# Performance work log

Hardware: AMD Instinct MI355X
Metric: run time of the kernel (lower is better)

The kernel has to match this reference:

```python
import jax, jax.numpy as jnp
import numpy as np

ROLLBACK = 1  # rollback_range: warp at 2**rollback finer resolution, then downsample
B, C, H, W = 2, 32, 512, 512
CIN = 3 * (C // 2) + 2  # inner module input channels


def _bilinear_warp(img, res):
    """Bilinear gather. img: [B,Cc,Hh,Ww]; res: [B,Hh,Ww,2] pixel offsets (x,y).
    Samples img at (x+res_x, y+res_y) with zero padding outside."""
    Bb, Cc, Hh, Ww = img.shape
    gy, gx = jnp.meshgrid(jnp.arange(Hh, dtype=img.dtype),
                          jnp.arange(Ww, dtype=img.dtype), indexing='ij')
    sx = gx[None] + res[..., 0]  # [B,Hh,Ww]
    sy = gy[None] + res[..., 1]
    x0 = jnp.floor(sx); y0 = jnp.floor(sy)
    wx = sx - x0; wy = sy - y0

    def gather(yi, xi):
        inb = ((yi >= 0) & (yi < Hh) & (xi >= 0) & (xi < Ww)).astype(img.dtype)
        yc = jnp.clip(yi, 0, Hh - 1).astype(jnp.int32)
        xc = jnp.clip(xi, 0, Ww - 1).astype(jnp.int32)
        v = jax.vmap(lambda im, y, x: im[:, y, x])(img, yc, xc)  # [B,Cc,Hh,Ww]
        return v * inb[:, None]

    v00 = gather(y0, x0);     v01 = gather(y0, x0 + 1)
    v10 = gather(y0 + 1, x0); v11 = gather(y0 + 1, x0 + 1)
    wx = wx[:, None]; wy = wy[:, None]  # broadcast over channels
    return (v00 * (1 - wy) * (1 - wx) + v01 * (1 - wy) * wx
            + v10 * wy * (1 - wx) + v11 * wy * wx)


def _resize_img(img, f):  # [B,Cc,Hh,Ww] bilinear spatial resize
    Bb, Cc, Hh, Ww = img.shape
    return jax.image.resize(img, (Bb, Cc, int(Hh * f), int(Ww * f)), 'bilinear')


def _resize_res(res, f):  # [B,Hh,Ww,2]; pixel-unit values scale with resolution
    Bb, Hh, Ww, _ = res.shape
    return jax.image.resize(res, (Bb, int(Hh * f), int(Ww * f), 2), 'bilinear') * f


def res_warp_img(img, res, rollback):
    if rollback > 0:
        f = 2 ** rollback
        out = _bilinear_warp(_resize_img(img, f), _resize_res(res, f))
        return _resize_img(out, 1.0 / f)
    return _bilinear_warp(img, res)


def res_warp_res(res_a, res_b, rollback):
    # warp residual field a (treated as a 2-channel image, values in pixel units) by b
    if rollback > 0:
        f = 2 ** rollback
        a = _resize_res(res_a, f); b = _resize_res(res_b, f)
        out = jnp.transpose(_bilinear_warp(jnp.transpose(a, (0, 3, 1, 2)), b), (0, 2, 3, 1))
        return _resize_res(out, 1.0 / f)
    out = _bilinear_warp(jnp.transpose(res_a, (0, 3, 1, 2)), res_b)
    return jnp.transpose(out, (0, 2, 3, 1))


def combine_residuals(res_a, res_b, rollback):
    # flow composition: apply a then b
    return res_b + res_warp_res(res_a, res_b, rollback)


def _conv3x3(x, w, b):
    y = jax.lax.conv_general_dilated(x, w, (1, 1), 'SAME',
                                     dimension_numbers=('NCHW', 'OIHW', 'NCHW'))
    return y + b[None, :, None, None]


def setup_inputs() -> dict:
    key = jax.random.key(0)
    k1, k2, k3 = jax.random.split(key, 3)
    x = jax.random.normal(k1, (B, C, H, W), dtype=jnp.float32)
    res = jax.random.normal(k2, (B, 2, H, W), dtype=jnp.float32)  # ~1px flow
    W_inner = jax.random.normal(k3, (2, CIN, 3, 3), dtype=jnp.float32) * 0.02
    b_inner = jnp.zeros((2,), dtype=jnp.float32)
    return {"x": x, "res": res, "W_inner": W_inner, "b_inner": b_inner, "level": 0}


def reference(x, res, W_inner, b_inner, level):
    res_hw = jnp.transpose(res, (0, 2, 3, 1))  # [B,H,W,2]
    nf = x.shape[1]
    src, tgt = x[:, :nf // 2], x[:, nf // 2:]
    warped_tgt = res_warp_img(tgt, res_hw, ROLLBACK)
    bundle = jnp.concatenate([src, tgt, warped_tgt, res], axis=1)  # [B,3C/2+2,H,W]
    adj = _conv3x3(bundle, W_inner, b_inner)  # hindsight_adjustment [B,2,H,W]
    # mode == 'combine_res': state['down'][level]['input'] = combined residual
    new_res = combine_residuals(res_hw, jnp.transpose(adj, (0, 2, 3, 1)), ROLLBACK)
    hindsight_warped_tgt = res_warp_img(tgt, new_res, ROLLBACK)
    return jnp.concatenate([src, hindsight_warped_tgt], axis=1)  # [B,C,H,W]
```

## Files before the change

### kernel.cpp

```cpp
#include <hip/hip_runtime.h>
#include <hip/hip_bf16.h>
#include <cstdint>
#include <cstddef>

#define HW   512
#define HW2  1024
#define SZ   (512 * 512)
#define NPT  (34 * 34)
#define K_PTS 5
#define SRCW 36
#define NSRC (SRCW * SRCW)
#define MARG 9

struct UpTap { int i0, i1; float w0, w1; };

__device__ __forceinline__ UpTap up_tap(int i) {
  UpTap t;
  int k = i >> 1;
  if ((i & 1) == 0) {
    t.i0 = k - 1; t.i1 = k; t.w0 = 0.25f; t.w1 = 0.75f;
    if (k == 0) { t.i0 = 0; t.w0 = 0.0f; t.w1 = 1.0f; }
  } else {
    t.i0 = k; t.i1 = k + 1; t.w0 = 0.75f; t.w1 = 0.25f;
    if (k == HW - 1) { t.i1 = HW - 1; t.w0 = 1.0f; t.w1 = 0.0f; }
  }
  return t;
}

__device__ __forceinline__ float up_at(const float* __restrict__ plane, int yi, int xi) {
  UpTap ty = up_tap(yi), tx = up_tap(xi);
  const float* r0 = plane + (size_t)ty.i0 * HW;
  const float* r1 = plane + (size_t)ty.i1 * HW;
  float v00 = r0[tx.i0], v01 = r0[tx.i1];
  float v10 = r1[tx.i0], v11 = r1[tx.i1];
  return ty.w0 * (tx.w0 * v00 + tx.w1 * v01) + ty.w1 * (tx.w0 * v10 + tx.w1 * v11);
}

__device__ __forceinline__ void axis_taps(float s, int& base, float& w0, float& w1, float& w2) {
  float f0 = floorf(s);
  int i0 = (int)f0;
  float fr = s - f0;
  int b = (i0 & 1) ? (i0 >> 1) : (i0 >> 1) - 1;
  b = b < 0 ? 0 : (b > (HW - 3) ? (HW - 3) : b);
  float w[3] = {0.0f, 0.0f, 0.0f};
  if ((unsigned)i0 < (unsigned)HW2) {
    UpTap t = up_tap(i0);
    w[t.i0 - b] += (1.0f - fr) * t.w0;
    w[t.i1 - b] += (1.0f - fr) * t.w1;
  }
  if ((unsigned)(i0 + 1) < (unsigned)HW2) {
    UpTap t = up_tap(i0 + 1);
    w[t.i0 - b] += fr * t.w0;
    w[t.i1 - b] += fr * t.w1;
  }
  base = b; w0 = w[0]; w1 = w[1]; w2 = w[2];
}

struct PtTaps {
  int   locoff;
  float wy0, wy1, wy2, wx0, wx1, wx2;
};

__device__ __forceinline__ void compute_taps(const float* __restrict__ fx,
                                             const float* __restrict__ fy,
                                             int gx0, int gy0, int xo, int yo, int tid,
                                             PtTaps (&pt)[K_PTS]) {
  #pragma unroll
  for (int i = 0; i < K_PTS; ++i) {
    int p = tid + i * 256;
    pt[i].locoff = 0;
    pt[i].wy0 = pt[i].wy1 = pt[i].wy2 = 0.0f;
    pt[i].wx0 = pt[i].wx1 = pt[i].wx2 = 0.0f;
    if (p < NPT) {
      int ry = p / 34, rx = p % 34;
      int yy = gy0 + ry, xx = gx0 + rx;
      if ((unsigned)yy < (unsigned)HW2 && (unsigned)xx < (unsigned)HW2) {
        float sx = (float)xx + 2.0f * up_at(fx, yy, xx);
        float sy = (float)yy + 2.0f * up_at(fy, yy, xx);
        int bx, by;
        axis_taps(sx, bx, pt[i].wx0, pt[i].wx1, pt[i].wx2);
        axis_taps(sy, by, pt[i].wy0, pt[i].wy1, pt[i].wy2);
        int rx_ = bx - xo, ry_ = by - yo;
        if ((unsigned)rx_ <= (unsigned)(SRCW - 3) && (unsigned)ry_ <= (unsigned)(SRCW - 3))
          pt[i].locoff = ry_ * SRCW + rx_;
        else
          pt[i].locoff = ~(by * HW + bx);
      }
    }
  }
}

__device__ __forceinline__ void stage_pair(const float* __restrict__ p0,
                                           const float* __restrict__ p1,
                                           float2* __restrict__ s_src,
                                           int xo, int yo, int tid) {
  #pragma unroll
  for (int i = 0; i < 6; ++i) {
    int p = tid + i * 256;
    if (p < NSRC) {
      int r = p / SRCW, c = p % SRCW;
      int gy = yo + r; gy = gy < 0 ? 0 : (gy > HW - 1 ? HW - 1 : gy);
      int gx = xo + c; gx = gx < 0 ? 0 : (gx > HW - 1 ? HW - 1 : gx);
      size_t o = (size_t)gy * HW + gx;
      s_src[p] = make_float2(p0[o], p1[o]);
    }
  }
}

__device__ __forceinline__ float eval3_global(const float* __restrict__ pl, int off, const PtTaps& t) {
  const float* p0 = pl + off;
  float r0 = t.wx0 * p0[0]        + t.wx1 * p0[1]          + t.wx2 * p0[2];
  float r1 = t.wx0 * p0[HW]       + t.wx1 * p0[HW + 1]     + t.wx2 * p0[HW + 2];
  float r2 = t.wx0 * p0[2 * HW]   + t.wx1 * p0[2 * HW + 1] + t.wx2 * p0[2 * HW + 2];
  return t.wy0 * r0 + t.wy1 * r1 + t.wy2 * r2;
}

__device__ __forceinline__ void eval_round(const float2* __restrict__ s_src,
                                           float2* __restrict__ s_tile,
                                           const float* __restrict__ plane0,
                                           const float* __restrict__ plane1,
                                           const PtTaps (&pt)[K_PTS], int tid) {
  #pragma unroll
  for (int i = 0; i < K_PTS; ++i) {
    int p = tid + i * 256;
    if (p < NPT) {
      const PtTaps t = pt[i];
      float a0, a1;
      if (t.locoff >= 0) {
        const float2* s = s_src + t.locoff;
        float2 v00 = s[0],        v01 = s[1],            v02 = s[2];
        float2 v10 = s[SRCW],     v11 = s[SRCW + 1],     v12 = s[SRCW + 2];
        float2 v20 = s[2 * SRCW], v21 = s[2 * SRCW + 1], v22 = s[2 * SRCW + 2];
        float r00 = t.wx0 * v00.x + t.wx1 * v01.x + t.wx2 * v02.x;
        float r10 = t.wx0 * v10.x + t.wx1 * v11.x + t.wx2 * v12.x;
        float r20 = t.wx0 * v20.x + t.wx1 * v21.x + t.wx2 * v22.x;
        float r01 = t.wx0 * v00.y + t.wx1 * v01.y + t.wx2 * v02.y;
        float r11 = t.wx0 * v10.y + t.wx1 * v11.y + t.wx2 * v12.y;
        float r21 = t.wx0 * v20.y + t.wx1 * v21.y + t.wx2 * v22.y;
        a0 = t.wy0 * r00 + t.wy1 * r10 + t.wy2 * r20;
        a1 = t.wy0 * r01 + t.wy1 * r11 + t.wy2 * r21;
      } else {
        int off = ~t.locoff;
        a0 = eval3_global(plane0, off, t);
        a1 = eval3_global(plane1, off, t);
      }
      s_tile[p] = make_float2(a0, a1);
    }
  }
}

__global__ void warp_img_kernel(const float* __restrict__ x,
                                const float* __restrict__ res,
                                float* __restrict__ out)
{
  __shared__ float2 s_src[NSRC];
  __shared__ float2 s_tile[NPT];

  const int b = blockIdx.z;
  const int tx0 = blockIdx.x * 16, ty0 = blockIdx.y * 16;
  const int gx0 = tx0 * 2 - 1, gy0 = ty0 * 2 - 1;
  const int xo = tx0 - MARG, yo = ty0 - MARG;
  const int tid = threadIdx.x;

  const float* resx = res + (size_t)b * 2 * SZ;
  const float* resy = resx + SZ;
  const float* tgt  = x + ((size_t)b * 32 + 16) * SZ;

  stage_pair(tgt, tgt + SZ, s_src, xo, yo, tid);

  PtTaps pt[K_PTS];
  compute_taps(resx, resy, gx0, gy0, xo, yo, tid, pt);

  const int ly = tid >> 4, lx = tid & 15;
  const int oy = ty0 + ly, ox = tx0 + lx;
  const float RW[4] = {0.25f, 0.75f, 0.75f, 0.25f};
  float wy[4], wx[4];
  float sumy = 0.f, sumx = 0.f;
  #pragma unroll
  for (int d = 0; d < 4; ++d) {
    int g = 2 * oy - 1 + d;
    wy[d] = ((unsigned)g < (unsigned)HW2) ? RW[d] : 0.0f; sumy += wy[d];
    g = 2 * ox - 1 + d;
    wx[d] = ((unsigned)g < (unsigned)HW2) ? RW[d] : 0.0f; sumx += wx[d];
  }
  const float inv = 1.0f / (sumy * sumx);

  __syncthreads();

  for (int c = 0; c < 16; c += 2) {
    const float* plane0 = tgt + (size_t)c * SZ;
    eval_round(s_src, s_tile, plane0, plane0 + SZ, pt, tid);
    __syncthreads();

    if (c < 14)
      stage_pair(plane0 + 2 * SZ, plane0 + 3 * SZ, s_src, xo, yo, tid);

    float acc0 = 0.0f, acc1 = 0.0f;
    #pragma unroll
    for (int dy = 0; dy < 4; ++dy) {
      float r0 = 0.0f, r1 = 0.0f;
      const int base = (2 * ly + dy) * 34 + 2 * lx;
      #pragma unroll
      for (int dx = 0; dx < 4; ++dx) {
        float2 v = s_tile[base + dx];
        r0 += wx[dx] * v.x;
        r1 += wx[dx] * v.y;
      }
      acc0 += wy[dy] * r0;
      acc1 += wy[dy] * r1;
    }
    size_t o = (((size_t)b * 32 + 16 + c) * HW + oy) * HW + ox;
    out[o] = acc0 * inv;
    out[o + SZ] = acc1 * inv;
    __syncthreads();
  }
}

#define CHN 18
#define CHE (CHN * CHN)

__global__ void __launch_bounds__(256)
conv_kernel(const float* __restrict__ x,
            const float* __restrict__ res,
            const float* __restrict__ Wc,
            const float* __restrict__ bc,
            float* __restrict__ out,
            float* __restrict__ adj)
{
  __shared__ float sw[900];
  __shared__ float sh[4][CHE];

  const int tid = threadIdx.x;
  for (int i = tid; i < 900; i += 256) sw[i] = Wc[i];

  const int b = blockIdx.z;
  const int tx0 = blockIdx.x * 16, ty0 = blockIdx.y * 16;
  const int ty = tid >> 4, tx = tid & 15;

  const float* px = x + (size_t)b * 32 * SZ;
  const float* pw = out + ((size_t)b * 32 + 16) * SZ;
  const float* pr = res + (size_t)b * 2 * SZ;

  const int ry0 = tid / CHN, rx0 = tid - ry0 * CHN;
  const int hy0 = ty0 - 1 + ry0, hx0 = tx0 - 1 + rx0;
  const bool ok0 = (unsigned)hy0 < (unsigned)HW && (unsigned)hx0 < (unsigned)HW;
  const int off0 = hy0 * HW + hx0;
  const int p1 = tid + 256;
  const bool sl1 = p1 < CHE;
  const int ry1 = p1 / CHN, rx1 = p1 - ry1 * CHN;
  const int hy1 = ty0 - 1 + ry1, hx1 = tx0 - 1 + rx1;
  const bool ok1 = sl1 && (unsigned)hy1 < (unsigned)HW && (unsigned)hx1 < (unsigned)HW;
  const int off1 = hy1 * HW + hx1;

  #define PLANE(ic) ((ic) < 32 ? px + (size_t)(ic) * SZ \
                   : (ic) < 48 ? pw + (size_t)((ic) - 32) * SZ \
                   : pr + (size_t)((ic) - 48) * SZ)

  float acc0 = bc[0];
  float acc1 = bc[1];

  {
    const float* plE = PLANE(0);
    const float* plO = PLANE(1);
    float e0 = ok0 ? plE[off0] : 0.f;
    float e1 = ok1 ? plE[off1] : 0.f;
    float o0 = ok0 ? plO[off0] : 0.f;
    float o1 = ok1 ? plO[off1] : 0.f;
    sh[0][tid] = e0; if (sl1) sh[0][p1] = e1;
    sh[1][tid] = o0; if (sl1) sh[1][p1] = o1;
  }

  const size_t pix = (size_t)(ty0 + ty) * HW + (tx0 + tx);

  for (int kk = 0; kk < 25; ++kk) {
    __syncthreads();
    float e0 = 0.f, e1 = 0.f, o0 = 0.f, o1 = 0.f;
    if (kk < 24) {
      const float* plE = PLANE(2 * kk + 2);
      const float* plO = PLANE(2 * kk + 3);
      e0 = ok0 ? plE[off0] : 0.f;
      e1 = ok1 ? plE[off1] : 0.f;
      o0 = ok0 ? plO[off0] : 0.f;
      o1 = ok1 ? plO[off1] : 0.f;
    }

    const int cur = (kk & 1) * 2;
    const float* hpE = sh[cur];
    const float* hpO = sh[cur + 1];
    const float* wE0 = &sw[(2 * kk) * 9];
    const float* wO0 = wE0 + 9;
    const float* wE1 = &sw[450 + (2 * kk) * 9];
    const float* wO1 = wE1 + 9;
    float cE = 0.f, cO = 0.f;
    #pragma unroll
    for (int ky = 0; ky < 3; ++ky) {
      #pragma unroll
      for (int kx = 0; kx < 3; ++kx) {
        float vE = hpE[(ty + ky) * CHN + tx + kx];
        float vO = hpO[(ty + ky) * CHN + tx + kx];
        if (ky == 1 && kx == 1) { cE = vE; cO = vO; }
        acc0 += vE * wE0[ky * 3 + kx];
        acc0 += vO * wO0[ky * 3 + kx];
        acc1 += vE * wE1[ky * 3 + kx];
        acc1 += vO * wO1[ky * 3 + kx];
      }
    }

    if (kk < 8) {
      size_t oc = ((size_t)b * 32 + 2 * kk) * SZ + pix;
      out[oc] = cE;
      out[oc + SZ] = cO;
    }

    if (kk < 24) {
      float* sE = sh[cur ^ 2];
      float* sO = sh[(cur ^ 2) + 1];
      sE[tid] = e0; if (sl1) sE[p1] = e1;
      sO[tid] = o0; if (sl1) sO[p1] = o1;
    }
  }
  #undef PLANE

  adj[((size_t)b * 2 + 0) * SZ + pix] = acc0;
  adj[((size_t)b * 2 + 1) * SZ + pix] = acc1;
}

__global__ void new_res_kernel(const float* __restrict__ res,
                               const float* __restrict__ adj,
                               float* __restrict__ nres)
{
  __shared__ float2 s_src[NSRC];
  __shared__ float2 s_tile[NPT];

  const int b = blockIdx.z;
  const int tx0 = blockIdx.x * 16, ty0 = blockIdx.y * 16;
  const int gx0 = tx0 * 2 - 1, gy0 = ty0 * 2 - 1;
  const int xo = tx0 - MARG, yo = ty0 - MARG;
  const int tid = threadIdx.x;

  const float* adjx = adj + (size_t)b * 2 * SZ;
  const float* adjy = adjx + SZ;
  const float* res0 = res + (size_t)b * 2 * SZ;
  const float* res1 = res0 + SZ;

  stage_pair(res0, res1, s_src, xo, yo, tid);

  PtTaps pt[K_PTS];
  compute_taps(adjx, adjy, gx0, gy0, xo, yo, tid, pt);

  const int ly = tid >> 4, lx = tid & 15;
  const int oy = ty0 + ly, ox = tx0 + lx;
  const float RW[4] = {0.25f, 0.75f, 0.75f, 0.25f};
  float wy[4], wx[4];
  float sumy = 0.f, sumx = 0.f;
  #pragma unroll
  for (int d = 0; d < 4; ++d) {
    int g = 2 * oy - 1 + d;
    wy[d] = ((unsigned)g < (unsigned)HW2) ? RW[d] : 0.0f; sumy += wy[d];
    g = 2 * ox - 1 + d;
    wx[d] = ((unsigned)g < (unsigned)HW2) ? RW[d] : 0.0f; sumx += wx[d];
  }
  const float inv = 1.0f / (sumy * sumx);

  __syncthreads();
  eval_round(s_src, s_tile, res0, res1, pt, tid);
  __syncthreads();

  float acc0 = 0.0f, acc1 = 0.0f;
  #pragma unroll
  for (int dy = 0; dy < 4; ++dy) {
    float r0 = 0.0f, r1 = 0.0f;
    const int base = (2 * ly + dy) * 34 + 2 * lx;
    #pragma unroll
    for (int dx = 0; dx < 4; ++dx) {
      float2 v = s_tile[base + dx];
      r0 += wx[dx] * v.x;
      r1 += wx[dx] * v.y;
    }
    acc0 += wy[dy] * r0;
    acc1 += wy[dy] * r1;
  }
  size_t o = ((size_t)b * 2) * SZ + (size_t)oy * HW + ox;
  nres[o]      = acc0 * inv + adjx[(size_t)oy * HW + ox];
  nres[o + SZ] = acc1 * inv + adjy[(size_t)oy * HW + ox];
}

extern "C" void kernel_launch(void* const* d_in, const int* in_sizes, int n_in,
                              void* d_out, int out_size, void* d_ws, size_t ws_size,
                              hipStream_t stream) {
  const float* x   = (const float*)d_in[0];
  const float* res = (const float*)d_in[1];
  const float* Wc  = (const float*)d_in[2];
  const float* bc  = (const float*)d_in[3];
  float* out = (float*)d_out;

  float* adj  = (float*)d_ws;
  float* nres = adj + (size_t)2 * 2 * SZ;

  dim3 tile_grid(32, 32, 2);

  warp_img_kernel<<<tile_grid, dim3(256), 0, stream>>>(x, res, out);

  conv_kernel<<<tile_grid, dim3(256), 0, stream>>>(x, res, Wc, bc, out, adj);

  new_res_kernel<<<tile_grid, dim3(256), 0, stream>>>(res, adj, nres);

  warp_img_kernel<<<tile_grid, dim3(256), 0, stream>>>(x, nres, out);
}
```

Measured before the change: 377.4 us.

## Stage flow field in LDS for tap computation and batch conv channels by four

```diff
diff --git a/kernel.cpp b/kernel.cpp
--- a/kernel.cpp
+++ b/kernel.cpp
@@ -11,6 +11,8 @@
 #define SRCW 36
 #define NSRC (SRCW * SRCW)
 #define MARG 9
+#define FDIM 18
+#define NFLD (FDIM * FDIM)
 
 struct UpTap { int i0, i1; float w0, w1; };
 
@@ -27,13 +29,17 @@
   return t;
 }
 
-__device__ __forceinline__ float up_at(const float* __restrict__ plane, int yi, int xi) {
+__device__ __forceinline__ float2 up_at2(const float2* __restrict__ f,
+                                         int yi, int xi, int oy, int ox) {
   UpTap ty = up_tap(yi), tx = up_tap(xi);
-  const float* r0 = plane + (size_t)ty.i0 * HW;
-  const float* r1 = plane + (size_t)ty.i1 * HW;
-  float v00 = r0[tx.i0], v01 = r0[tx.i1];
-  float v10 = r1[tx.i0], v11 = r1[tx.i1];
-  return ty.w0 * (tx.w0 * v00 + tx.w1 * v01) + ty.w1 * (tx.w0 * v10 + tx.w1 * v11);
+  const float2* r0 = f + (ty.i0 - oy) * FDIM - ox;
+  const float2* r1 = f + (ty.i1 - oy) * FDIM - ox;
+  float2 v00 = r0[tx.i0], v01 = r0[tx.i1];
+  float2 v10 = r1[tx.i0], v11 = r1[tx.i1];
+  float2 r;
+  r.x = ty.w0 * (tx.w0 * v00.x + tx.w1 * v01.x) + ty.w1 * (tx.w0 * v10.x + tx.w1 * v11.x);
+  r.y = ty.w0 * (tx.w0 * v00.y + tx.w1 * v01.y) + ty.w1 * (tx.w0 * v10.y + tx.w1 * v11.y);
+  return r;
 }
 
 __device__ __forceinline__ void axis_taps(float s, int& base, float& w0, float& w1, float& w2) {
@@ -61,8 +67,25 @@
   float wy0, wy1, wy2, wx0, wx1, wx2;
 };
 
-__device__ __forceinline__ void compute_taps(const float* __restrict__ fx,
-                                             const float* __restrict__ fy,
+__device__ __forceinline__ void stage_field(const float* __restrict__ fx,
+                                            const float* __restrict__ fy,
+                                            float2* __restrict__ sf,
+                                            int fy0, int fx0, int tid) {
+  #pragma unroll
+  for (int i = 0; i < 2; ++i) {
+    int p = tid + i * 256;
+    if (p < NFLD) {
+      int r = p / FDIM, c = p % FDIM;
+      int gy = fy0 + r; gy = gy < 0 ? 0 : (gy > HW - 1 ? HW - 1 : gy);
+      int gx = fx0 + c; gx = gx < 0 ? 0 : (gx > HW - 1 ? HW - 1 : gx);
+      size_t o = (size_t)gy * HW + gx;
+      sf[p] = make_float2(fx[o], fy[o]);
+    }
+  }
+}
+
+__device__ __forceinline__ void compute_taps(const float2* __restrict__ sf,
+                                             int fy0, int fx0,
                                              int gx0, int gy0, int xo, int yo, int tid,
                                              PtTaps (&pt)[K_PTS]) {
   #pragma unroll
@@ -75,8 +98,9 @@
       int ry = p / 34, rx = p % 34;
       int yy = gy0 + ry, xx = gx0 + rx;
       if ((unsigned)yy < (unsigned)HW2 && (unsigned)xx < (unsigned)HW2) {
-        float sx = (float)xx + 2.0f * up_at(fx, yy, xx);
-        float sy = (float)yy + 2.0f * up_at(fy, yy, xx);
+        float2 d = up_at2(sf, yy, xx, fy0, fx0);
+        float sx = (float)xx + 2.0f * d.x;
+        float sy = (float)yy + 2.0f * d.y;
         int bx, by;
         axis_taps(sx, bx, pt[i].wx0, pt[i].wx1, pt[i].wx2);
         axis_taps(sy, by, pt[i].wy0, pt[i].wy1, pt[i].wy2);
@@ -160,6 +184,7 @@
   const int tx0 = blockIdx.x * 16, ty0 = blockIdx.y * 16;
   const int gx0 = tx0 * 2 - 1, gy0 = ty0 * 2 - 1;
   const int xo = tx0 - MARG, yo = ty0 - MARG;
+  const int fy0 = ty0 - 1, fx0 = tx0 - 1;
   const int tid = threadIdx.x;
 
   const float* resx = res + (size_t)b * 2 * SZ;
@@ -167,9 +192,7 @@
   const float* tgt  = x + ((size_t)b * 32 + 16) * SZ;
 
   stage_pair(tgt, tgt + SZ, s_src, xo, yo, tid);
-
-  PtTaps pt[K_PTS];
-  compute_taps(resx, resy, gx0, gy0, xo, yo, tid, pt);
+  stage_field(resx, resy, s_tile, fy0, fx0, tid);
 
   const int ly = tid >> 4, lx = tid & 15;
   const int oy = ty0 + ly, ox = tx0 + lx;
@@ -184,6 +207,11 @@
     wx[d] = ((unsigned)g < (unsigned)HW2) ? RW[d] : 0.0f; sumx += wx[d];
   }
   const float inv = 1.0f / (sumy * sumx);
+
+  __syncthreads();
+
+  PtTaps pt[K_PTS];
+  compute_taps(s_tile, fy0, fx0, gx0, gy0, xo, yo, tid, pt);
 
   __syncthreads();
 
@@ -228,7 +256,7 @@
             float* __restrict__ adj)
 {
   __shared__ float sw[900];
-  __shared__ float sh[4][CHE];
+  __shared__ float sh[8][CHE];
 
   const int tid = threadIdx.x;
   for (int i = tid; i < 900; i += 256) sw[i] = Wc[i];
@@ -259,64 +287,94 @@
   float acc0 = bc[0];
   float acc1 = bc[1];
 
+  float q0[4], q1[4];
   {
-    const float* plE = PLANE(0);
-    const float* plO = PLANE(1);
-    float e0 = ok0 ? plE[off0] : 0.f;
-    float e1 = ok1 ? plE[off1] : 0.f;
-    float o0 = ok0 ? plO[off0] : 0.f;
-    float o1 = ok1 ? plO[off1] : 0.f;
-    sh[0][tid] = e0; if (sl1) sh[0][p1] = e1;
-    sh[1][tid] = o0; if (sl1) sh[1][p1] = o1;
+    #pragma unroll
+    for (int j = 0; j < 4; ++j) {
+      const float* pl = PLANE(j);
+      q0[j] = ok0 ? pl[off0] : 0.f;
+      q1[j] = ok1 ? pl[off1] : 0.f;
+    }
+    #pragma unroll
+    for (int j = 0; j < 4; ++j) {
+      sh[j][tid] = q0[j];
+      if (sl1) sh[j][p1] = q1[j];
+    }
   }
 
   const size_t pix = (size_t)(ty0 + ty) * HW + (tx0 + tx);
 
-  for (int kk = 0; kk < 25; ++kk) {
+  for (int kk = 0; kk < 12; ++kk) {
     __syncthreads();
-    float e0 = 0.f, e1 = 0.f, o0 = 0.f, o1 = 0.f;
-    if (kk < 24) {
-      const float* plE = PLANE(2 * kk + 2);
-      const float* plO = PLANE(2 * kk + 3);
-      e0 = ok0 ? plE[off0] : 0.f;
-      e1 = ok1 ? plE[off1] : 0.f;
-      o0 = ok0 ? plO[off0] : 0.f;
-      o1 = ok1 ? plO[off1] : 0.f;
-    }
-
-    const int cur = (kk & 1) * 2;
-    const float* hpE = sh[cur];
-    const float* hpO = sh[cur + 1];
-    const float* wE0 = &sw[(2 * kk) * 9];
-    const float* wO0 = wE0 + 9;
-    const float* wE1 = &sw[450 + (2 * kk) * 9];
-    const float* wO1 = wE1 + 9;
-    float cE = 0.f, cO = 0.f;
+    if (kk < 11) {
+      #pragma unroll
+      for (int j = 0; j < 4; ++j) {
+        const float* pl = PLANE(4 * kk + 4 + j);
+        q0[j] = ok0 ? pl[off0] : 0.f;
+        q1[j] = ok1 ? pl[off1] : 0.f;
+      }
+    } else {
+      #pragma unroll
+      for (int j = 0; j < 2; ++j) {
+        const float* pl = PLANE(48 + j);
+        q0[j] = ok0 ? pl[off0] : 0.f;
+        q1[j] = ok1 ? pl[off1] : 0.f;
+      }
+    }
+
+    const int cur = (kk & 1) * 4;
+    float cen[4];
     #pragma unroll
     for (int ky = 0; ky < 3; ++ky) {
       #pragma unroll
       for (int kx = 0; kx < 3; ++kx) {
-        float vE = hpE[(ty + ky) * CHN + tx + kx];
-        float vO = hpO[(ty + ky) * CHN + tx + kx];
-        if (ky == 1 && kx == 1) { cE = vE; cO = vO; }
-        acc0 += vE * wE0[ky * 3 + kx];
-        acc0 += vO * wO0[ky * 3 + kx];
-        acc1 += vE * wE1[ky * 3 + kx];
-        acc1 += vO * wO1[ky * 3 + kx];
-      }
-    }
-
-    if (kk < 8) {
-      size_t oc = ((size_t)b * 32 + 2 * kk) * SZ + pix;
-      out[oc] = cE;
-      out[oc + SZ] = cO;
-    }
-
-    if (kk < 24) {
-      float* sE = sh[cur ^ 2];
-      float* sO = sh[(cur ^ 2) + 1];
-      sE[tid] = e0; if (sl1) sE[p1] = e1;
-      sO[tid] = o0; if (sl1) sO[p1] = o1;
+        const int hoff = (ty + ky) * CHN + tx + kx;
+        const int widx = ky * 3 + kx;
+        #pragma unroll
+        for (int j = 0; j < 4; ++j) {
+          float v = sh[cur + j][hoff];
+          if (ky == 1 && kx == 1) cen[j] = v;
+          acc0 += v * sw[(4 * kk + j) * 9 + widx];
+          acc1 += v * sw[450 + (4 * kk + j) * 9 + widx];
+        }
+      }
+    }
+
+    if (kk < 4) {
+      #pragma unroll
+      for (int j = 0; j < 4; ++j)
+        out[((size_t)b * 32 + 4 * kk + j) * SZ + pix] = cen[j];
+    }
+
+    const int nxt = cur ^ 4;
+    if (kk < 11) {
+      #pragma unroll
+      for (int j = 0; j < 4; ++j) {
+        sh[nxt + j][tid] = q0[j];
+        if (sl1) sh[nxt + j][p1] = q1[j];
+      }
+    } else {
+      #pragma unroll
+      for (int j = 0; j < 2; ++j) {
+        sh[nxt + j][tid] = q0[j];
+        if (sl1) sh[nxt + j][p1] = q1[j];
+      }
+    }
+  }
+
+  __syncthreads();
+  #pragma unroll
+  for (int ky = 0; ky < 3; ++ky) {
+    #pragma unroll
+    for (int kx = 0; kx < 3; ++kx) {
+      const int hoff = (ty + ky) * CHN + tx + kx;
+      const int widx = ky * 3 + kx;
+      #pragma unroll
+      for (int j = 0; j < 2; ++j) {
+        float v = sh[j][hoff];
+        acc0 += v * sw[(48 + j) * 9 + widx];
+        acc1 += v * sw[450 + (48 + j) * 9 + widx];
+      }
     }
   }
   #undef PLANE
@@ -336,6 +394,7 @@
   const int tx0 = blockIdx.x * 16, ty0 = blockIdx.y * 16;
   const int gx0 = tx0 * 2 - 1, gy0 = ty0 * 2 - 1;
   const int xo = tx0 - MARG, yo = ty0 - MARG;
+  const int fy0 = ty0 - 1, fx0 = tx0 - 1;
   const int tid = threadIdx.x;
 
   const float* adjx = adj + (size_t)b * 2 * SZ;
@@ -344,9 +403,7 @@
   const float* res1 = res0 + SZ;
 
   stage_pair(res0, res1, s_src, xo, yo, tid);
-
-  PtTaps pt[K_PTS];
-  compute_taps(adjx, adjy, gx0, gy0, xo, yo, tid, pt);
+  stage_field(adjx, adjy, s_tile, fy0, fx0, tid);
 
   const int ly = tid >> 4, lx = tid & 15;
   const int oy = ty0 + ly, ox = tx0 + lx;
@@ -363,6 +420,12 @@
   const float inv = 1.0f / (sumy * sumx);
 
   __syncthreads();
+
+  PtTaps pt[K_PTS];
+  compute_taps(s_tile, fy0, fx0, gx0, gy0, xo, yo, tid, pt);
+
+  __syncthreads();
+
   eval_round(s_src, s_tile, res0, res1, pt, tid);
   __syncthreads();
 
```

After: 371.8 us. Within noise of the previous version (-1.5%).
